# Kernel optimization log

Hardware: AMD Instinct MI355X
Metric: run time of the kernel (lower is better)

The kernel has to match this reference:

```python
import jax, jax.numpy as jnp
import numpy as np

VOCAB = 32000; DIM = 512; NL = 6; B = 2; L = 1024
DI = 2 * DIM      # d_inner (expand=2)
DS = 16           # d_state
DC = 4            # d_conv
DR = DIM // 16    # dt_rank = ceil(512/16) = 32


def setup_inputs() -> dict:
    key = jax.random.key(0)
    ks = jax.random.split(key, 10)
    s = 0.02
    tokens = jax.random.randint(ks[0], (B, L), 0, VOCAB)
    pos_emb = jax.random.normal(ks[1], (1, L, DIM)) * s
    embed = jax.random.normal(ks[2], (VOCAB, DIM)) * s
    lm_w = jax.random.normal(ks[3], (VOCAB, DIM)) * s
    lm_b = jnp.zeros((VOCAB,), jnp.float32)
    in_proj_w = jax.random.normal(ks[4], (NL, 2 * DI, DIM)) * s
    conv_w = jax.random.normal(ks[5], (NL, DI, DC)) * s
    conv_b = jnp.zeros((NL, DI), jnp.float32)
    x_proj_w = jax.random.normal(ks[6], (NL, DR + 2 * DS, DI)) * s
    dt_proj_w = jax.random.normal(ks[7], (NL, DI, DR)) * s
    dt_proj_b = jnp.broadcast_to(jnp.log(jnp.expm1(jnp.float32(0.01))), (NL, DI)).astype(jnp.float32)
    A_log = jnp.log(jnp.broadcast_to(jnp.arange(1, DS + 1, dtype=jnp.float32), (NL, DI, DS)))
    Dp = jnp.ones((NL, DI), jnp.float32)
    out_w = jax.random.normal(ks[8], (NL, DIM, DI)) * s
    ln_g = jnp.ones((NL, DIM), jnp.float32)
    ln_b = jnp.zeros((NL, DIM), jnp.float32)
    return dict(tokens=tokens, pos_emb=pos_emb, embed=embed, lm_w=lm_w, lm_b=lm_b,
                in_proj_w=in_proj_w, conv_w=conv_w, conv_b=conv_b, x_proj_w=x_proj_w,
                dt_proj_w=dt_proj_w, dt_proj_b=dt_proj_b, A_log=A_log, Dp=Dp,
                out_w=out_w, ln_g=ln_g, ln_b=ln_b)


def silu(x):
    return x * jax.nn.sigmoid(x)


def layernorm(x, g, b, eps=1e-5):
    mu = jnp.mean(x, -1, keepdims=True)
    var = jnp.var(x, -1, keepdims=True)
    return (x - mu) * jax.lax.rsqrt(var + eps) * g + b


def causal_dwconv(x, w, b):
    # x: (B,L,DI), w: (DI,DC) depthwise, left-pad causal
    xp = jnp.pad(x, ((0, 0), (DC - 1, 0), (0, 0)))
    y = b
    for k in range(DC):
        y = y + w[:, k] * xp[:, k:k + x.shape[1], :]
    return y


def selective_scan(u, dt, A, Bm, Cm, Dp):
    # u,dt: (B,L,DI); A: (DI,DS); Bm,Cm: (B,L,DS)
    dA = jnp.exp(dt[..., None] * A)                       # (B,L,DI,DS)
    dBu = dt[..., None] * Bm[:, :, None, :] * u[..., None]
    h0 = jnp.zeros((u.shape[0], DI, DS), u.dtype)

    def step(h, inp):
        dA_t, dBu_t, C_t = inp
        h = dA_t * h + dBu_t
        y = jnp.einsum('bdn,bn->bd', h, C_t)
        return h, y

    _, ys = jax.lax.scan(step, h0, (dA.transpose(1, 0, 2, 3),
                                    dBu.transpose(1, 0, 2, 3),
                                    Cm.transpose(1, 0, 2)))
    return ys.transpose(1, 0, 2) + u * Dp


def mamba_block(x, in_w, cw, cb, xp_w, dtw, dtb, A_log, Dp, ow):
    xz = jnp.einsum('bld,ed->ble', x, in_w)               # (B,L,2*DI)
    xc, z = jnp.split(xz, 2, axis=-1)
    xc = silu(causal_dwconv(xc, cw, cb))
    x_dbl = jnp.einsum('bld,ed->ble', xc, xp_w)           # (B,L,DR+2*DS)
    dt, Bm, Cm = jnp.split(x_dbl, [DR, DR + DS], axis=-1)
    dt = jax.nn.softplus(jnp.einsum('blr,dr->bld', dt, dtw) + dtb)
    A = -jnp.exp(A_log)
    y = selective_scan(xc, dt, A, Bm, Cm, Dp)
    y = y * silu(z)
    return jnp.einsum('bld,ed->ble', y, ow)


def reference(tokens, pos_emb, embed, lm_w, lm_b, in_proj_w, conv_w, conv_b,
              x_proj_w, dt_proj_w, dt_proj_b, A_log, Dp, out_w, ln_g, ln_b):
    x = embed[tokens] + pos_emb[:, :tokens.shape[1]]
    for i in range(NL):
        res = x
        x = mamba_block(x, in_proj_w[i], conv_w[i], conv_b[i], x_proj_w[i],
                        dt_proj_w[i], dt_proj_b[i], A_log[i], Dp[i], out_w[i])
        x = layernorm(x + res, ln_g[i], ln_b[i])
    return jnp.einsum('bld,vd->blv', x, lm_w) + lm_b
```

## Files before the change

### kernel.cpp

```cpp
#include <hip/hip_runtime.h>
#include <hip/hip_bf16.h>
#include <math.h>

#define BB 2
#define LL 1024
#define DIM 512
#define NL 6
#define DI 1024
#define DS 16
#define DC 4
#define DR 32
#define VOCAB 32000
#define M_ROWS (BB * LL)
#define CCH 64
#define CHLEN (LL / CCH)
#define KSPLIT 8
#define OSPLIT 2

typedef unsigned short u16;
typedef __attribute__((ext_vector_type(8))) short bf16x8;
typedef __attribute__((ext_vector_type(4))) float f32x4;

__device__ __forceinline__ u16 f2bf(float f) {
    unsigned u = __float_as_uint(f);
    u += 0x7FFF + ((u >> 16) & 1);
    return (u16)(u >> 16);
}
__device__ __forceinline__ float bf2f(u16 h) {
    return __uint_as_float(((unsigned)h) << 16);
}
#define SWZ(r, c) ((c) ^ (((r) >> 1) & 3))

__global__ __launch_bounds__(256) void cast_all(const float* __restrict__ lm,
                                                const float* __restrict__ inw,
                                                const float* __restrict__ ow,
                                                const float* __restrict__ xp,
                                                u16* __restrict__ lmb,
                                                u16* __restrict__ inb,
                                                u16* __restrict__ owb_,
                                                u16* __restrict__ xpb) {
    int idx = blockIdx.x * 256 + threadIdx.x;
    const float* src; u16* dst; int off;
    if (idx < 2048000)      { src = lm;  dst = lmb;  off = idx; }
    else if (idx < 2834432) { src = inw; dst = inb;  off = idx - 2048000; }
    else if (idx < 3227648) { src = ow;  dst = owb_; off = idx - 2834432; }
    else                    { src = xp;  dst = xpb;  off = idx - 3227648; }
    float4 v0 = ((const float4*)src)[off * 2];
    float4 v1 = ((const float4*)src)[off * 2 + 1];
    union { u16 h[8]; int4 v; } r;
    r.h[0] = f2bf(v0.x); r.h[1] = f2bf(v0.y); r.h[2] = f2bf(v0.z); r.h[3] = f2bf(v0.w);
    r.h[4] = f2bf(v1.x); r.h[5] = f2bf(v1.y); r.h[6] = f2bf(v1.z); r.h[7] = f2bf(v1.w);
    ((int4*)dst)[off] = r.v;
}

__global__ __launch_bounds__(256) void embed_kernel(const int* __restrict__ tok,
                                                    const float* __restrict__ pos,
                                                    const float* __restrict__ emb,
                                                    float* __restrict__ x,
                                                    u16* __restrict__ xb) {
    int idx = blockIdx.x * 256 + threadIdx.x;
    int d = idx & (DIM - 1);
    int l = (idx >> 9) & (LL - 1);
    int b = idx >> 19;
    int t = tok[b * LL + l];
    float v = emb[(size_t)t * DIM + d] + pos[l * DIM + d];
    x[idx] = v;
    xb[idx] = f2bf(v);
}

__global__ __launch_bounds__(256) void gemm_n64(const u16* __restrict__ A,
                                                const u16* __restrict__ W,
                                                float* __restrict__ out,
                                                u16* __restrict__ outb,
                                                const float* __restrict__ bias,
                                                int lda, int ldw, int ldc,
                                                int KS, int pstride) {
    __shared__ __align__(16) char smem_raw[36864];
    u16* As = (u16*)smem_raw;
    u16* Ws = (u16*)(smem_raw + 24576);
    float* Cs = (float*)smem_raw;

    const int t = threadIdx.x;
    const int l = t & 63;
    const int w = t >> 6;
    const int gx = gridDim.x, gy = gridDim.y;
    const int nwg = gx * gy * gridDim.z;
    const int fid = (blockIdx.z * gy + blockIdx.y) * gx + blockIdx.x;
    const int q8 = nwg >> 3, r8 = nwg & 7;
    const int xcd = fid & 7, rank = fid >> 3;
    const int wgid = (xcd < r8 ? xcd * (q8 + 1) : r8 * (q8 + 1) + (xcd - r8) * q8) + rank;
    const int kz = wgid % gx;
    const int bm = ((wgid / gx) % gy) * 128;
    const int bnn = (wgid / (gx * gy)) * 64;
    const int wm = w * 32;

    f32x4 acc[2][4] = {};
    const int nt = KS >> 5;
    const int kbeg = kz * KS;

    auto STAGE = [&](int bufi, int k0) {
#pragma unroll
        for (int p = 0; p < 2; ++p) {
            const int i = p * 256 + w * 64 + l;
            const int row = i >> 2;
            const int kq = SWZ(row, i & 3);
            __builtin_amdgcn_global_load_lds(
                (const __attribute__((address_space(1))) unsigned int*)
                    (A + (size_t)(bm + row) * lda + k0 + kq * 8),
                (__attribute__((address_space(3))) unsigned int*)
                    (As + bufi * 4096 + (p * 256 + w * 64) * 8),
                16, 0, 0);
        }
        {
            const int i = w * 64 + l;
            const int row = i >> 2;
            const int kq = SWZ(row, i & 3);
            __builtin_amdgcn_global_load_lds(
                (const __attribute__((address_space(1))) unsigned int*)
                    (W + (size_t)(bnn + row) * ldw + k0 + kq * 8),
                (__attribute__((address_space(3))) unsigned int*)
                    (Ws + bufi * 2048 + (w * 64) * 8),
                16, 0, 0);
        }
    };
    auto COMPUTE = [&](int bufi) {
        const u16* Ab = As + bufi * 4096;
        const u16* Wb = Ws + bufi * 2048;
        bf16x8 bfr[4];
#pragma unroll
        for (int ni = 0; ni < 4; ++ni) {
            const int wr = ni * 16 + (l & 15);
            bfr[ni] = *(const bf16x8*)(Wb + wr * 32 + SWZ(wr, l >> 4) * 8);
        }
#pragma unroll
        for (int mi = 0; mi < 2; ++mi) {
            const int ar = wm + mi * 16 + (l & 15);
            bf16x8 a = *(const bf16x8*)(Ab + ar * 32 + SWZ(ar, l >> 4) * 8);
#pragma unroll
            for (int ni = 0; ni < 4; ++ni)
                acc[mi][ni] = __builtin_amdgcn_mfma_f32_16x16x32_bf16(bfr[ni], a, acc[mi][ni], 0, 0, 0);
        }
    };

    STAGE(0, kbeg);
    if (nt == 1) {
        asm volatile("s_waitcnt vmcnt(0)\ns_barrier" ::: "memory");
        COMPUTE(0);
        asm volatile("s_waitcnt lgkmcnt(0)" ::: "memory");
    } else {
        STAGE(1, kbeg + 32);
        int b0 = 0;
        for (int tt = 0; tt < nt - 2; ++tt) {
            int b2 = b0 + 2; if (b2 >= 3) b2 -= 3;
            STAGE(b2, kbeg + ((tt + 2) << 5));
            asm volatile("s_waitcnt vmcnt(6)\ns_barrier" ::: "memory");
            COMPUTE(b0);
            asm volatile("s_waitcnt lgkmcnt(0)\ns_barrier" ::: "memory");
            ++b0; if (b0 == 3) b0 = 0;
        }
        asm volatile("s_waitcnt vmcnt(3)\ns_barrier" ::: "memory");
        COMPUTE(b0);
        asm volatile("s_waitcnt lgkmcnt(0)\ns_barrier" ::: "memory");
        ++b0; if (b0 == 3) b0 = 0;
        asm volatile("s_waitcnt vmcnt(0)\ns_barrier" ::: "memory");
        COMPUTE(b0);
        asm volatile("s_waitcnt lgkmcnt(0)" ::: "memory");
    }

    if (outb != nullptr) {
        u16* opb = outb + (size_t)kz * pstride;
#pragma unroll
        for (int mi = 0; mi < 2; ++mi) {
            const int row = bm + wm + mi * 16 + (l & 15);
#pragma unroll
            for (int ni = 0; ni < 4; ++ni) {
                const int col = bnn + ni * 16 + ((l >> 4) << 2);
                ushort4 v;
                v.x = f2bf(acc[mi][ni][0]); v.y = f2bf(acc[mi][ni][1]);
                v.z = f2bf(acc[mi][ni][2]); v.w = f2bf(acc[mi][ni][3]);
                *(ushort4*)(opb + (size_t)row * ldc + col) = v;
            }
        }
    } else {
        float* op = out + (size_t)kz * pstride;
        __syncthreads();
#pragma unroll
        for (int pass = 0; pass < 2; ++pass) {
            if ((w >> 1) == pass) {
                const int rbase = (w & 1) * 32;
#pragma unroll
                for (int mi = 0; mi < 2; ++mi) {
                    const int r = rbase + mi * 16 + (l & 15);
#pragma unroll
                    for (int ni = 0; ni < 4; ++ni) {
                        const int c = ni * 16 + ((l >> 4) << 2);
                        float4 v;
                        v.x = acc[mi][ni][0]; v.y = acc[mi][ni][1];
                        v.z = acc[mi][ni][2]; v.w = acc[mi][ni][3];
                        *(float4*)(Cs + r * 65 + c) = v;
                    }
                }
            }
            __syncthreads();
#pragma unroll
            for (int it = 0; it < 4; ++it) {
                const int idx = it * 256 + t;
                const int r = idx >> 4;
                const int c4 = (idx & 15) * 4;
                float4 v = *(float4*)(Cs + r * 65 + c4);
                if (bias != nullptr) {
                    float4 b4 = *(const float4*)(bias + bnn + c4);
                    v.x += b4.x; v.y += b4.y; v.z += b4.z; v.w += b4.w;
                }
                *(float4*)(op + (size_t)(bm + pass * 64 + r) * ldc + bnn + c4) = v;
            }
            __syncthreads();
        }
    }
}

__global__ __launch_bounds__(256) void conv_silu(const u16* __restrict__ xzb,
                                                 const float* __restrict__ cw,
                                                 const float* __restrict__ cb,
                                                 u16* __restrict__ xcb) {
    int idx8 = blockIdx.x * 256 + threadIdx.x;
    int c0 = (idx8 & 127) * 8;
    int m = idx8 >> 7;
    int l = m & (LL - 1);

    float acc[8];
    float4 cb0 = *(const float4*)(cb + c0);
    float4 cb1 = *(const float4*)(cb + c0 + 4);
    acc[0] = cb0.x; acc[1] = cb0.y; acc[2] = cb0.z; acc[3] = cb0.w;
    acc[4] = cb1.x; acc[5] = cb1.y; acc[6] = cb1.z; acc[7] = cb1.w;
#pragma unroll
    for (int k = 0; k < DC; ++k) {
        int ll = l + k - (DC - 1);
        if (ll < 0) continue;
        const u16* row = xzb + ((size_t)(m + k - (DC - 1))) * (2 * DI) + c0;
        ushort4 r0 = *(const ushort4*)row;
        ushort4 r1 = *(const ushort4*)(row + 4);
#pragma unroll
        for (int j = 0; j < 4; ++j) {
            acc[j]     += cw[(c0 + j) * DC + k]     * bf2f(((const u16*)&r0)[j]);
            acc[j + 4] += cw[(c0 + j + 4) * DC + k] * bf2f(((const u16*)&r1)[j]);
        }
    }
    ushort4 o0, o1;
#pragma unroll
    for (int j = 0; j < 4; ++j) {
        float v0 = acc[j]     / (1.f + __expf(-acc[j]));
        float v1 = acc[j + 4] / (1.f + __expf(-acc[j + 4]));
        ((u16*)&o0)[j] = f2bf(v0);
        ((u16*)&o1)[j] = f2bf(v1);
    }
    u16* op = xcb + (size_t)idx8 * 8;
    *(ushort4*)op = o0;
    *(ushort4*)(op + 4) = o1;
}

__global__ __launch_bounds__(256) void scan_pass1(const u16* __restrict__ xcb,
                                                  const float* __restrict__ Pf,
                                                  const float* __restrict__ dtw,
                                                  const float* __restrict__ dtb,
                                                  const float* __restrict__ A_log,
                                                  float* __restrict__ S,
                                                  float* __restrict__ Q) {
    __shared__ float xds[CHLEN][64];
    const int t = threadIdx.x;
    const int d = blockIdx.x * 256 + t;
    const int b = blockIdx.y;
    const int c = blockIdx.z;
    const int l0 = c * CHLEN;
    const int m0 = b * LL + l0;

    for (int i = t; i < CHLEN * 64; i += 256) {
        int r = i >> 6, cc = i & 63;
        float s = 0.f;
#pragma unroll
        for (int kz = 0; kz < KSPLIT; ++kz)
            s += Pf[(size_t)kz * (M_ROWS * 64) + (m0 + r) * 64 + cc];
        xds[r][cc] = s;
    }
    __syncthreads();

    float4 wreg[8];
#pragma unroll
    for (int kk = 0; kk < 8; ++kk)
        wreg[kk] = *(const float4*)(dtw + (size_t)d * DR + kk * 4);
    const float dtbv = dtb[d];

    float a[DS];
#pragma unroll
    for (int q = 0; q < 4; ++q) {
        float4 al = *(const float4*)(A_log + d * DS + q * 4);
        a[q * 4 + 0] = -__expf(al.x);
        a[q * 4 + 1] = -__expf(al.y);
        a[q * 4 + 2] = -__expf(al.z);
        a[q * 4 + 3] = -__expf(al.w);
    }
    float Qr[DS];
#pragma unroll
    for (int n = 0; n < DS; ++n) Qr[n] = 0.f;
    float Ssum = 0.f;

    const u16* up = xcb + (size_t)m0 * DI + d;

    for (int l = 0; l < CHLEN; ++l) {
        float dacc = dtbv;
#pragma unroll
        for (int kk = 0; kk < 8; ++kk) {
            float4 xv = *(const float4*)&xds[l][kk * 4];
            dacc += wreg[kk].x * xv.x + wreg[kk].y * xv.y +
                    wreg[kk].z * xv.z + wreg[kk].w * xv.w;
        }
        float dtv = (dacc > 20.f) ? dacc : log1pf(__expf(dacc));
        float uv = bf2f(up[(size_t)l * DI]);
        float wv = dtv * uv;
        Ssum += dtv;
#pragma unroll
        for (int q = 0; q < 4; ++q) {
            float4 Bv = *(const float4*)&xds[l][32 + q * 4];
            float dA0 = __expf(dtv * a[q * 4 + 0]);
            float dA1 = __expf(dtv * a[q * 4 + 1]);
            float dA2 = __expf(dtv * a[q * 4 + 2]);
            float dA3 = __expf(dtv * a[q * 4 + 3]);
            Qr[q * 4 + 0] = dA0 * Qr[q * 4 + 0] + wv * Bv.x;
            Qr[q * 4 + 1] = dA1 * Qr[q * 4 + 1] + wv * Bv.y;
            Qr[q * 4 + 2] = dA2 * Qr[q * 4 + 2] + wv * Bv.z;
            Qr[q * 4 + 3] = dA3 * Qr[q * 4 + 3] + wv * Bv.w;
        }
    }
    S[((size_t)b * CCH + c) * DI + d] = Ssum;
    float* Qp = Q + (((size_t)b * CCH + c) * DI + d) * DS;
#pragma unroll
    for (int q = 0; q < 4; ++q) {
        float4 o;
        o.x = Qr[q * 4 + 0]; o.y = Qr[q * 4 + 1];
        o.z = Qr[q * 4 + 2]; o.w = Qr[q * 4 + 3];
        *(float4*)(Qp + q * 4) = o;
    }
}

__global__ __launch_bounds__(64) void scan_pass2(const float* __restrict__ A_log,
                                                 const float* __restrict__ S,
                                                 float* __restrict__ Q) {
    const int idx = blockIdx.x * 64 + threadIdx.x;
    const int b = idx >> 14;
    const int dn = idx & 16383;
    const int d = dn >> 4;
    const float a = -__expf(A_log[dn]);
    float h = 0.f;
    for (int c = 0; c < CCH; ++c) {
        const size_t soff = ((size_t)b * CCH + c) * DI + d;
        const size_t qoff = ((size_t)b * CCH + c) * (size_t)(DI * DS) + dn;
        float P = __expf(a * S[soff]);
        float qv = Q[qoff];
        Q[qoff] = h;
        h = P * h + qv;
    }
}

__global__ __launch_bounds__(256) void scan_pass3(const u16* __restrict__ xcb,
                                                  const float* __restrict__ Pf,
                                                  const float* __restrict__ dtw,
                                                  const float* __restrict__ dtb,
                                                  const u16* __restrict__ xzb,
                                                  const float* __restrict__ A_log,
                                                  const float* __restrict__ Dpp,
                                                  const float* __restrict__ Q,
                                                  u16* __restrict__ y) {
    __shared__ float xds[CHLEN][64];
    const int t = threadIdx.x;
    const int d = blockIdx.x * 256 + t;
    const int b = blockIdx.y;
    const int c = blockIdx.z;
    const int l0 = c * CHLEN;
    const int m0 = b * LL + l0;

    for (int i = t; i < CHLEN * 64; i += 256) {
        int r = i >> 6, cc = i & 63;
        float s = 0.f;
#pragma unroll
        for (int kz = 0; kz < KSPLIT; ++kz)
            s += Pf[(size_t)kz * (M_ROWS * 64) + (m0 + r) * 64 + cc];
        xds[r][cc] = s;
    }
    __syncthreads();

    float4 wreg[8];
#pragma unroll
    for (int kk = 0; kk < 8; ++kk)
        wreg[kk] = *(const float4*)(dtw + (size_t)d * DR + kk * 4);
    const float dtbv = dtb[d];

    float a[DS];
#pragma unroll
    for (int q = 0; q < 4; ++q) {
        float4 al = *(const float4*)(A_log + d * DS + q * 4);
        a[q * 4 + 0] = -__expf(al.x);
        a[q * 4 + 1] = -__expf(al.y);
        a[q * 4 + 2] = -__expf(al.z);
        a[q * 4 + 3] = -__expf(al.w);
    }
    float h[DS];
    const float* Qp = Q + (((size_t)b * CCH + c) * DI + d) * DS;
#pragma unroll
    for (int q = 0; q < 4; ++q) {
        float4 hv = *(const float4*)(Qp + q * 4);
        h[q * 4 + 0] = hv.x; h[q * 4 + 1] = hv.y;
        h[q * 4 + 2] = hv.z; h[q * 4 + 3] = hv.w;
    }
    const float dp = Dpp[d];

    const u16* up = xcb + (size_t)m0 * DI + d;
    const u16* zp = xzb + (size_t)m0 * (2 * DI) + DI + d;
    u16* yp = y + (size_t)m0 * DI + d;

    for (int l = 0; l < CHLEN; ++l) {
        float dacc = dtbv;
#pragma unroll
        for (int kk = 0; kk < 8; ++kk) {
            float4 xv = *(const float4*)&xds[l][kk * 4];
            dacc += wreg[kk].x * xv.x + wreg[kk].y * xv.y +
                    wreg[kk].z * xv.z + wreg[kk].w * xv.w;
        }
        float dtv = (dacc > 20.f) ? dacc : log1pf(__expf(dacc));
        float uv = bf2f(up[(size_t)l * DI]);
        float wv = dtv * uv;
        float p = 0.f;
#pragma unroll
        for (int q = 0; q < 4; ++q) {
            float4 Bv = *(const float4*)&xds[l][32 + q * 4];
            float4 Cv = *(const float4*)&xds[l][48 + q * 4];
            float dA0 = __expf(dtv * a[q * 4 + 0]);
            float dA1 = __expf(dtv * a[q * 4 + 1]);
            float dA2 = __expf(dtv * a[q * 4 + 2]);
            float dA3 = __expf(dtv * a[q * 4 + 3]);
            h[q * 4 + 0] = dA0 * h[q * 4 + 0] + wv * Bv.x;
            h[q * 4 + 1] = dA1 * h[q * 4 + 1] + wv * Bv.y;
            h[q * 4 + 2] = dA2 * h[q * 4 + 2] + wv * Bv.z;
            h[q * 4 + 3] = dA3 * h[q * 4 + 3] + wv * Bv.w;
            p += h[q * 4 + 0] * Cv.x + h[q * 4 + 1] * Cv.y +
                 h[q * 4 + 2] * Cv.z + h[q * 4 + 3] * Cv.w;
        }
        float zv = bf2f(zp[(size_t)l * (2 * DI)]);
        float g = zv / (1.f + __expf(-zv));
        yp[(size_t)l * DI] = f2bf((p + uv * dp) * g);
    }
}

__global__ __launch_bounds__(256) void add_ln(const float* __restrict__ opart,
                                              float* __restrict__ x,
                                              const float* __restrict__ g,
                                              const float* __restrict__ b,
                                              u16* __restrict__ xb) {
    const int PS = M_ROWS * DIM;
    int m = blockIdx.x;
    int t = threadIdx.x;
    const float* xr = x + (size_t)m * DIM;
    float v0 = xr[t];
    float v1 = xr[t + 256];
#pragma unroll
    for (int kz = 0; kz < OSPLIT; ++kz) {
        const float* op = opart + (size_t)kz * PS + (size_t)m * DIM;
        v0 += op[t];
        v1 += op[t + 256];
    }
    float s = v0 + v1;
    float ss = v0 * v0 + v1 * v1;
#pragma unroll
    for (int off = 32; off > 0; off >>= 1) {
        s += __shfl_down(s, off, 64);
        ss += __shfl_down(ss, off, 64);
    }
    __shared__ float sb[4], ssb[4];
    int w = t >> 6;
    if ((t & 63) == 0) { sb[w] = s; ssb[w] = ss; }
    __syncthreads();
    float stot = sb[0] + sb[1] + sb[2] + sb[3];
    float sstot = ssb[0] + ssb[1] + ssb[2] + ssb[3];
    float mean = stot * (1.f / DIM);
    float var = sstot * (1.f / DIM) - mean * mean;
    float rs = rsqrtf(var + 1e-5f);
    float* xw = x + (size_t)m * DIM;
    float o0 = (v0 - mean) * rs * g[t] + b[t];
    float o1 = (v1 - mean) * rs * g[t + 256] + b[t + 256];
    xw[t] = o0;
    xw[t + 256] = o1;
    xb[(size_t)m * DIM + t] = f2bf(o0);
    xb[(size_t)m * DIM + t + 256] = f2bf(o1);
}

extern "C" void kernel_launch(void* const* d_in, const int* in_sizes, int n_in,
                              void* d_out, int out_size, void* d_ws, size_t ws_size,
                              hipStream_t stream) {
    const int*   tokens = (const int*)d_in[0];
    const float* pos    = (const float*)d_in[1];
    const float* emb    = (const float*)d_in[2];
    const float* lm_w   = (const float*)d_in[3];
    const float* lm_b   = (const float*)d_in[4];
    const float* in_w   = (const float*)d_in[5];
    const float* cw     = (const float*)d_in[6];
    const float* cb     = (const float*)d_in[7];
    const float* xpw    = (const float*)d_in[8];
    const float* dtw    = (const float*)d_in[9];
    const float* dtb    = (const float*)d_in[10];
    const float* A_log  = (const float*)d_in[11];
    const float* Dpp    = (const float*)d_in[12];
    const float* ow     = (const float*)d_in[13];
    const float* lng    = (const float*)d_in[14];
    const float* lnb    = (const float*)d_in[15];
    float* out = (float*)d_out;

    float* ws = (float*)d_ws;
    float* x    = ws;
    float* S    = x + 1048576;
    float* Qb   = S + 131072;
    float* Pf   = Qb + 2097152;
    float* Pf2  = Pf + 1048576;
    u16* xzb    = (u16*)(Pf2 + 2097152);
    u16* xb     = xzb + 4194304;
    u16* yb     = xb + 1048576;
    u16* xcb    = yb + 2097152;
    u16* lm_wb  = xcb + 2097152;
    u16* in_wb  = lm_wb + 16384000;
    u16* owb    = in_wb + 6291456;
    u16* xpwb   = owb + 3145728;

    cast_all<<<12800, 256, 0, stream>>>(lm_w, in_w, ow, xpw,
                                        lm_wb, in_wb, owb, xpwb);

    embed_kernel<<<M_ROWS * DIM / 256, 256, 0, stream>>>(tokens, pos, emb, x, xb);

    for (int i = 0; i < NL; ++i) {
        gemm_n64<<<dim3(1, M_ROWS / 128, 2048 / 64), 256, 0, stream>>>(
            xb, in_wb + (size_t)i * 2048 * 512, nullptr, xzb, nullptr,
            512, 512, 2048, 512, 0);
        conv_silu<<<M_ROWS * DI / 8 / 256, 256, 0, stream>>>(
            xzb, cw + (size_t)i * DI * DC, cb + (size_t)i * DI, xcb);
        gemm_n64<<<dim3(KSPLIT, M_ROWS / 128, 1), 256, 0, stream>>>(
            xcb, xpwb + (size_t)i * 64 * 1024, Pf, nullptr, nullptr,
            1024, 1024, 64, 1024 / KSPLIT, M_ROWS * 64);
        scan_pass1<<<dim3(DI / 256, BB, CCH), 256, 0, stream>>>(
            xcb, Pf, dtw + (size_t)i * DI * DR, dtb + (size_t)i * DI,
            A_log + (size_t)i * DI * DS, S, Qb);
        scan_pass2<<<(BB * DI * DS) / 64, 64, 0, stream>>>(
            A_log + (size_t)i * DI * DS, S, Qb);
        scan_pass3<<<dim3(DI / 256, BB, CCH), 256, 0, stream>>>(
            xcb, Pf, dtw + (size_t)i * DI * DR, dtb + (size_t)i * DI, xzb,
            A_log + (size_t)i * DI * DS, Dpp + (size_t)i * DI, Qb, yb);
        gemm_n64<<<dim3(OSPLIT, M_ROWS / 128, 512 / 64), 256, 0, stream>>>(
            yb, owb + (size_t)i * 512 * 1024, Pf2, nullptr, nullptr,
            1024, 1024, 512, 1024 / OSPLIT, M_ROWS * 512);
        add_ln<<<M_ROWS, 256, 0, stream>>>(
            Pf2, x, lng + (size_t)i * DIM, lnb + (size_t)i * DIM, xb);
    }

    gemm_n64<<<dim3(1, M_ROWS / 128, VOCAB / 64), 256, 0, stream>>>(
        xb, lm_wb, out, nullptr, lm_b,
        512, 512, VOCAB, 512, 0);
}
```

Measured before the change: 826.4 us.

## Add 256x256-tile GEMM kernel for LM head with XCD-aware block mapping

Replaces the 128x64-tile GEMM used for the vocabulary projection with a new 512-thread kernel that computes 256x256 output tiles. It uses a triple-buffered global-to-LDS pipeline and an XCD-aware workgroup remap so blocks sharing weight columns land on the same XCD. The epilogue stages results through LDS in four passes, adds the bias and writes float4 rows. The larger tile raises arithmetic intensity and cuts redundant reloads of A and W, but uses 96KB of LDS and many accumulators, which lowers occupancy.

```diff
diff --git a/kernel.cpp b/kernel.cpp
--- a/kernel.cpp
+++ b/kernel.cpp
@@ -68,6 +68,129 @@
     xb[idx] = f2bf(v);
 }
 
+__global__ __launch_bounds__(512) void gemm_256(const u16* __restrict__ A,
+                                                const u16* __restrict__ W,
+                                                float* __restrict__ C,
+                                                const float* __restrict__ bias,
+                                                int K, int N) {
+    __shared__ __align__(16) char smem_raw[98304];
+    u16* As = (u16*)smem_raw;
+    u16* Ws = (u16*)(smem_raw + 49152);
+    float* Cs = (float*)smem_raw;
+
+    const int t = threadIdx.x;
+    const int l = t & 63;
+    const int w = t >> 6;
+    const int wr = w >> 2;
+    const int wc = w & 3;
+
+    const int nwg = gridDim.x;
+    const int q8 = nwg >> 3, r8 = nwg & 7;
+    const int xcd = blockIdx.x & 7, rank = blockIdx.x >> 3;
+    const int wgid = (xcd < r8 ? xcd * (q8 + 1) : r8 * (q8 + 1) + (xcd - r8) * q8) + rank;
+    const int bm = (wgid & 7) * 256;
+    const int bn = (wgid >> 3) * 256;
+
+    f32x4 acc[8][4] = {};
+    const int nt = K >> 5;
+
+    auto STAGE = [&](int bufi, int k0) {
+#pragma unroll
+        for (int p = 0; p < 2; ++p) {
+            const int g = p * 512 + t;
+            const int row = g >> 2, slot = g & 3;
+            __builtin_amdgcn_global_load_lds(
+                (const __attribute__((address_space(1))) unsigned int*)
+                    (A + (size_t)(bm + row) * K + k0 + SWZ(row, slot) * 8),
+                (__attribute__((address_space(3))) unsigned int*)
+                    (As + bufi * 8192 + (p * 512 + w * 64) * 8),
+                16, 0, 0);
+        }
+#pragma unroll
+        for (int p = 0; p < 2; ++p) {
+            const int g = p * 512 + t;
+            const int row = g >> 2, slot = g & 3;
+            __builtin_amdgcn_global_load_lds(
+                (const __attribute__((address_space(1))) unsigned int*)
+                    (W + (size_t)(bn + row) * K + k0 + SWZ(row, slot) * 8),
+                (__attribute__((address_space(3))) unsigned int*)
+                    (Ws + bufi * 8192 + (p * 512 + w * 64) * 8),
+                16, 0, 0);
+        }
+    };
+    auto COMPUTE = [&](int bufi) {
+        const u16* Ab = As + bufi * 8192;
+        const u16* Wb = Ws + bufi * 8192;
+        bf16x8 bfr[4];
+#pragma unroll
+        for (int ni = 0; ni < 4; ++ni) {
+            const int wrow = wc * 64 + ni * 16 + (l & 15);
+            bfr[ni] = *(const bf16x8*)(Wb + wrow * 32 + SWZ(wrow, l >> 4) * 8);
+        }
+#pragma unroll
+        for (int mi = 0; mi < 8; ++mi) {
+            const int arow = wr * 128 + mi * 16 + (l & 15);
+            bf16x8 a = *(const bf16x8*)(Ab + arow * 32 + SWZ(arow, l >> 4) * 8);
+#pragma unroll
+            for (int ni = 0; ni < 4; ++ni)
+                acc[mi][ni] = __builtin_amdgcn_mfma_f32_16x16x32_bf16(bfr[ni], a, acc[mi][ni], 0, 0, 0);
+        }
+    };
+
+    STAGE(0, 0);
+    STAGE(1, 32);
+    int b0 = 0;
+    for (int tt = 0; tt < nt - 2; ++tt) {
+        int b2 = b0 + 2; if (b2 >= 3) b2 -= 3;
+        STAGE(b2, (tt + 2) << 5);
+        asm volatile("s_waitcnt vmcnt(8)\ns_barrier" ::: "memory");
+        COMPUTE(b0);
+        asm volatile("s_waitcnt lgkmcnt(0)\ns_barrier" ::: "memory");
+        ++b0; if (b0 == 3) b0 = 0;
+    }
+    asm volatile("s_waitcnt vmcnt(4)\ns_barrier" ::: "memory");
+    COMPUTE(b0);
+    asm volatile("s_waitcnt lgkmcnt(0)\ns_barrier" ::: "memory");
+    ++b0; if (b0 == 3) b0 = 0;
+    asm volatile("s_waitcnt vmcnt(0)\ns_barrier" ::: "memory");
+    COMPUTE(b0);
+    asm volatile("s_waitcnt lgkmcnt(0)" ::: "memory");
+    __syncthreads();
+
+#pragma unroll
+    for (int pass = 0; pass < 4; ++pass) {
+        if (wr == (pass >> 1)) {
+            const int pm0 = (pass & 1) * 4;
+#pragma unroll
+            for (int mi2 = 0; mi2 < 4; ++mi2) {
+                const int r = mi2 * 16 + (l & 15);
+#pragma unroll
+                for (int ni = 0; ni < 4; ++ni) {
+                    const int c = wc * 64 + ni * 16 + ((l >> 4) << 2);
+                    float4 v;
+                    v.x = acc[pm0 + mi2][ni][0]; v.y = acc[pm0 + mi2][ni][1];
+                    v.z = acc[pm0 + mi2][ni][2]; v.w = acc[pm0 + mi2][ni][3];
+                    *(float4*)(Cs + r * 260 + c) = v;
+                }
+            }
+        }
+        __syncthreads();
+#pragma unroll
+        for (int it = 0; it < 8; ++it) {
+            const int idx = it * 512 + t;
+            const int r = idx >> 6;
+            const int c4 = (idx & 63) * 4;
+            float4 v = *(float4*)(Cs + r * 260 + c4);
+            if (bias != nullptr) {
+                float4 b4 = *(const float4*)(bias + bn + c4);
+                v.x += b4.x; v.y += b4.y; v.z += b4.z; v.w += b4.w;
+            }
+            *(float4*)(C + (size_t)(bm + pass * 64 + r) * N + bn + c4) = v;
+        }
+        __syncthreads();
+    }
+}
+
 __global__ __launch_bounds__(256) void gemm_n64(const u16* __restrict__ A,
                                                 const u16* __restrict__ W,
                                                 float* __restrict__ out,
@@ -129,8 +252,8 @@
         bf16x8 bfr[4];
 #pragma unroll
         for (int ni = 0; ni < 4; ++ni) {
-            const int wr = ni * 16 + (l & 15);
-            bfr[ni] = *(const bf16x8*)(Wb + wr * 32 + SWZ(wr, l >> 4) * 8);
+            const int wr2 = ni * 16 + (l & 15);
+            bfr[ni] = *(const bf16x8*)(Wb + wr2 * 32 + SWZ(wr2, l >> 4) * 8);
         }
 #pragma unroll
         for (int mi = 0; mi < 2; ++mi) {
@@ -557,7 +680,6 @@
             Pf2, x, lng + (size_t)i * DIM, lnb + (size_t)i * DIM, xb);
     }
 
-    gemm_n64<<<dim3(1, M_ROWS / 128, VOCAB / 64), 256, 0, stream>>>(
-        xb, lm_wb, out, nullptr, lm_b,
-        512, 512, VOCAB, 512, 0);
-}
+    gemm_256<<<(M_ROWS / 256) * (VOCAB / 256), 512, 0, stream>>>(
+        xb, lm_wb, out, lm_b, 512, VOCAB);
+}
```

Result: faster. 794.5 us (-3.9%).
